# Kernel optimization log

Measured on AMD Instinct MI355X. Metric: run time of the kernel, lower is better.

The kernel has to match this reference:

```python
import jax, jax.numpy as jnp
import numpy as np

RARITY_ALPHA = 0.5


def _forward(obs_emb, observed_mask, lengths, avg_interval, var_prior_emb_tensor,
             rarity_W, adjI, p2s_W1, p2s_b1, p2s_W2, p2s_b2,
             Wu, bu, Wr, br, Wc, bc):
    B, T, N, D = obs_emb.shape
    I = jnp.eye(N, dtype=obs_emb.dtype)
    # hypernetwork conditioning vector per node (prior_to_state MLP); identical
    # across batch since var_prior_emb_tensor is repeated over the batch dim.
    vv = jax.nn.relu(var_prior_emb_tensor @ p2s_W1 + p2s_b1) @ p2s_W2 + p2s_b2  # [N,E]
    vv = jnp.broadcast_to(vv[None], (B, N, vv.shape[-1]))                        # [B,N,E]
    tot = observed_mask.sum(axis=1)  # var_total_obs [B,N]

    def gate(z, W, b):
        # MLP_Param: per-node weights W_n = sum_e vv[n,e]*W[e]; fused einsum avoids
        # materializing [B,N,2D+1,D].
        return jnp.einsum('bni,bne,eio->bno', z, vv, W) + jnp.einsum('bne,eo->bno', vv, b)

    def step_fn(carry, xs):
        h, out = carry
        cur_obs, m, cur_avg, step = xs  # [B,N,D], [B,N], [B,N], scalar
        rs = RARITY_ALPHA * jnp.tanh(cur_avg / (tot + 1.0))                  # [B,N]
        rmat = -rarity_W * jnp.abs(rs[:, :, None] - rs[:, None, :])          # [B,N,N]
        # adj_mask[b,i,j] = observed(b,i)*observed(b,j)  (column-set then row-zero)
        adj_mask = m[:, :, None] * m[:, None, :]
        cur_adj = adjI * (1.0 + rmat) * adj_mask * (1.0 - I) + I             # [B,N,N]
        x = jnp.concatenate([cur_obs, rs[..., None]], axis=-1)              # [B,N,D+1]
        comb = jnp.einsum('bij,bjf->bif', cur_adj,
                          jnp.concatenate([x, h], axis=-1))                  # [B,N,2D+1]
        r = jax.nn.sigmoid(gate(comb, Wr, br))
        u = jax.nn.sigmoid(gate(comb, Wu, bu))
        mm = m[..., None] > 0
        h1 = jnp.where(mm, r * h, h)                      # h[nodes_ind] = r*h[nodes_ind]
        cand = jnp.tanh(gate(jnp.concatenate([x, h1], axis=-1), Wc, bc))
        h2 = jnp.where(mm, (1.0 - u) * h1 + u * cand, h1)  # scatter back at observed nodes
        out = jnp.where((step == lengths - 1)[:, None, None], h2, out)
        return (h2, out), None

    h0 = jnp.zeros((B, N, D), obs_emb.dtype)
    xs = (obs_emb.transpose(1, 0, 2, 3), observed_mask.transpose(1, 0, 2),
          avg_interval.transpose(1, 0, 2), jnp.arange(T))
    (_, out), _ = jax.lax.scan(step_fn, (h0, jnp.zeros_like(h0)), xs)
    return out


def setup_inputs() -> dict:
    B, T, N, D, E = 32, 64, 128, 64, 5
    key = jax.random.key(0)
    ks = jax.random.split(key, 18)
    inp = {}
    inp['obs_emb'] = jax.random.normal(ks[0], (B, T, N, D), jnp.float32)
    inp['adj'] = jax.random.normal(ks[1], (N, N), jnp.float32)  # unused by forward
    inp['observed_mask'] = (jax.random.uniform(ks[2], (B, T, N)) < 0.5).astype(jnp.float32)
    inp['observed_tp'] = jax.random.uniform(ks[3], (B, T), jnp.float32)       # unused
    inp['tp_emb_tensor'] = jax.random.normal(ks[4], (B, T, 1), jnp.float32)   # unused
    inp['lengths'] = jax.random.randint(ks[5], (B,), T // 2, T + 1, jnp.int32)
    inp['avg_interval'] = jax.random.uniform(ks[6], (B, T, N), jnp.float32)
    inp['var_prior_emb_tensor'] = jax.random.normal(ks[7], (N, 768), jnp.float32)
    # learned parameters
    inp['rarity_W'] = jax.random.normal(ks[8], (N, N), jnp.float32)
    inp['adjI'] = jnp.eye(N, dtype=jnp.float32) + 0.01 * jax.random.normal(ks[9], (N, N), jnp.float32)
    inp['p2s_W1'] = 0.05 * jax.random.normal(ks[10], (768, 2 * D), jnp.float32)
    inp['p2s_b1'] = jnp.zeros((2 * D,), jnp.float32)
    inp['p2s_W2'] = 0.1 * jax.random.normal(ks[11], (2 * D, E), jnp.float32)
    inp['p2s_b2'] = jnp.zeros((E,), jnp.float32)
    inp['Wu'] = 0.1 * jax.random.normal(ks[12], (E, 2 * D + 1, D), jnp.float32)
    inp['bu'] = 0.1 * jax.random.normal(ks[13], (E, D), jnp.float32)
    inp['Wr'] = 0.1 * jax.random.normal(ks[14], (E, 2 * D + 1, D), jnp.float32)
    inp['br'] = 0.1 * jax.random.normal(ks[15], (E, D), jnp.float32)
    inp['Wc'] = 0.1 * jax.random.normal(ks[16], (E, 2 * D + 1, D), jnp.float32)
    inp['bc'] = 0.1 * jax.random.normal(ks[17], (E, D), jnp.float32)
    return inp


def reference(obs_emb, adj, observed_mask, observed_tp, tp_emb_tensor, lengths,
              avg_interval, var_prior_emb_tensor, rarity_W, adjI, p2s_W1, p2s_b1,
              p2s_W2, p2s_b2, Wu, bu, Wr, br, Wc, bc):
    # adj, observed_tp, tp_emb_tensor are accepted but never used, as in the torch code
    return _forward(obs_emb, observed_mask, lengths, avg_interval, var_prior_emb_tensor,
                    rarity_W, adjI, p2s_W1, p2s_b1, p2s_W2, p2s_b2,
                    Wu, bu, Wr, br, Wc, bc)
```

## Files before the change

kernel.cpp:

```cpp
#include <hip/hip_runtime.h>
#include <math.h>

constexpr size_t WS_VV  = 1024;
constexpr size_t WS_TOT = 2048;
constexpr size_t WS_RS  = 8192;
constexpr size_t WS_WH  = 270336;
constexpr size_t WS_WX  = 1843200;
constexpr size_t WS_BF  = 3440640;
constexpr size_t WS_H   = 3465216;
constexpr size_t CXSZ   = 2129920;
constexpr size_t GXSZ   = 2097152;
constexpr size_t WS_CX0 = 3727360;
constexpr size_t WS_GXR0= 7987200;
constexpr size_t WS_GXU0= 12181504;
constexpr size_t WS_CXC0= 16375808;

__device__ __forceinline__ float sigm(float x){ return 1.f/(1.f+expf(-x)); }

__device__ __forceinline__ float2 ld2_mall(const float* p){
  union { unsigned long long u; float2 f; } cv;
  cv.u = __hip_atomic_load((const unsigned long long*)p, __ATOMIC_RELAXED,
                           __HIP_MEMORY_SCOPE_AGENT);
  return cv.f;
}
__device__ __forceinline__ void st2_mall(float* p, float a, float b){
  union { unsigned long long u; float2 f; } cv;
  cv.f = make_float2(a, b);
  __hip_atomic_store((unsigned long long*)p, cv.u, __ATOMIC_RELAXED,
                     __HIP_MEMORY_SCOPE_AGENT);
}

__global__ void k_vv(const float* __restrict__ vpe, const float* __restrict__ W1,
                     const float* __restrict__ b1, const float* __restrict__ W2,
                     const float* __restrict__ b2, float* __restrict__ ws){
  int n = blockIdx.x, tid = threadIdx.x;
  __shared__ float hid[128];
  if (tid < 128){
    float acc = b1[tid];
    for (int k=0;k<768;k++) acc = fmaf(vpe[n*768+k], W1[k*128+tid], acc);
    hid[tid] = fmaxf(acc, 0.f);
  }
  __syncthreads();
  if (tid < 5){
    float acc = b2[tid];
    for (int h=0;h<128;h++) acc = fmaf(hid[h], W2[h*5+tid], acc);
    ws[WS_VV + n*5 + tid] = acc;
  }
}

__global__ void k_fold(const float* __restrict__ Wr, const float* __restrict__ Wu,
                       const float* __restrict__ Wc, const float* __restrict__ br,
                       const float* __restrict__ bu, const float* __restrict__ bc,
                       float* __restrict__ ws){
  int bid = blockIdx.x; int g = bid>>7; int n = bid&127;
  const float* W  = (g==0)?Wr:(g==1)?Wu:Wc;
  const float* bb = (g==0)?br:(g==1)?bu:bc;
  float v[5];
#pragma unroll
  for (int e=0;e<5;e++) v[e] = ws[WS_VV + n*5 + e];
  for (int idx=threadIdx.x; idx<129*64; idx+=256){
    int i = idx>>6, o = idx&63;
    float a = 0.f;
#pragma unroll
    for (int e=0;e<5;e++) a = fmaf(v[e], W[(e*129+i)*64+o], a);
    if (i < 65) ws[WS_WX + (size_t)(g*128+n)*4160 + i*64 + o] = a;
    else        ws[WS_WH + (size_t)(g*128+n)*4096 + (i-65)*64 + o] = a;
  }
  if (threadIdx.x < 64){
    int o = threadIdx.x; float a = 0.f;
#pragma unroll
    for (int e=0;e<5;e++) a = fmaf(v[e], bb[e*64+o], a);
    ws[WS_BF + (g*128+n)*64 + o] = a;
  }
}

__global__ void k_tot(const float* __restrict__ mask, float* __restrict__ ws){
  int id = blockIdx.x*256 + threadIdx.x;
  int b = id>>7, n = id&127;
  float s = 0.f;
  for (int t=0;t<64;t++) s += mask[(b*64+t)*128 + n];
  ws[WS_TOT + b*128 + n] = s;
}

__global__ void k_rs(const float* __restrict__ avg, float* __restrict__ ws){
  int id = blockIdx.x*256 + threadIdx.x;
  int b = id>>13, n = id&127;
  float tot = ws[WS_TOT + b*128 + n];
  ws[WS_RS + id] = 0.5f * tanhf(avg[id] / (tot + 1.f));
}

__device__ void p4a_body(float* smem, const float* __restrict__ obs,
      const float* __restrict__ mask, const float* __restrict__ adjI,
      const float* __restrict__ rW, const int* __restrict__ lengths,
      float* __restrict__ ws, int cc, int rc){
  int b = rc>>3, tl = rc&7, t = cc*8 + tl;
  if (t >= lengths[b]) return;
  int rt = b*64 + t;
  float* xt   = smem;
  float* adjh = smem + 4352;
  float* rs_l = smem + 13056;
  float* m_l  = smem + 13184;
  int tid = threadIdx.x;
  if (tid < 128){ rs_l[tid] = ws[WS_RS + rt*128 + tid]; m_l[tid] = mask[rt*128 + tid]; }
  __syncthreads();
  int it = tid>>3, ft = tid&7, i0 = it*4, f0 = ft*8;
  float4 aL[4], aH[4]; float a64[4];
#pragma unroll
  for (int ii=0;ii<4;ii++){ aL[ii]=make_float4(0,0,0,0); aH[ii]=make_float4(0,0,0,0); a64[ii]=0.f; }
  for (int half=0; half<2; half++){
    __syncthreads();
    int j0 = half*64;
    for (int idx=tid; idx<4096; idx+=256){
      int jl = idx>>6, f = idx&63;
      xt[jl*68+f] = obs[(size_t)rt*8192 + (j0+jl)*64 + f];
    }
    if (tid < 64) xt[tid*68+64] = rs_l[j0+tid];
    for (int idx=tid; idx<8192; idx+=256){
      int i = idx>>6, jl = idx&63, j = j0+jl;
      float a;
      if (i == j) a = 1.f;
      else {
        int gi = i*128 + j;
        float dd = fabsf(rs_l[i] - rs_l[j]);
        a = adjI[gi] * (1.f - rW[gi]*dd) * m_l[i] * m_l[j];
      }
      adjh[i*68+jl] = a;
    }
    __syncthreads();
    for (int jb=0; jb<16; jb++){
      float4 av[4];
#pragma unroll
      for (int ii=0;ii<4;ii++) av[ii] = *(const float4*)&adjh[(i0+ii)*68 + jb*4];
#pragma unroll
      for (int jj=0;jj<4;jj++){
        int jl = jb*4 + jj;
        float4 xlo = *(const float4*)&xt[jl*68 + f0];
        float4 xhi = *(const float4*)&xt[jl*68 + f0 + 4];
        float xr = xt[jl*68 + 64];
#pragma unroll
        for (int ii=0;ii<4;ii++){
          float a = (jj==0)?av[ii].x:(jj==1)?av[ii].y:(jj==2)?av[ii].z:av[ii].w;
          aL[ii].x = fmaf(a, xlo.x, aL[ii].x); aL[ii].y = fmaf(a, xlo.y, aL[ii].y);
          aL[ii].z = fmaf(a, xlo.z, aL[ii].z); aL[ii].w = fmaf(a, xlo.w, aL[ii].w);
          aH[ii].x = fmaf(a, xhi.x, aH[ii].x); aH[ii].y = fmaf(a, xhi.y, aH[ii].y);
          aH[ii].z = fmaf(a, xhi.z, aH[ii].z); aH[ii].w = fmaf(a, xhi.w, aH[ii].w);
          a64[ii] = fmaf(a, xr, a64[ii]);
        }
      }
    }
  }
  size_t cxb = WS_CX0 + (size_t)(cc&1)*CXSZ;
#pragma unroll
  for (int ii=0;ii<4;ii++){
    int i = i0 + ii;
    size_t base = cxb + (size_t)i*16640 + (size_t)rc*65 + f0;
    ws[base+0]=aL[ii].x; ws[base+1]=aL[ii].y; ws[base+2]=aL[ii].z; ws[base+3]=aL[ii].w;
    ws[base+4]=aH[ii].x; ws[base+5]=aH[ii].y; ws[base+6]=aH[ii].z; ws[base+7]=aH[ii].w;
    if (ft == 0) ws[cxb + (size_t)i*16640 + (size_t)rc*65 + 64] = a64[ii];
  }
}

__device__ void p4b_body(float* smem, const float* __restrict__ obs,
      const int* __restrict__ lengths, float* __restrict__ ws, int cc, int pbid){
  if (pbid >= 768) return;
  int g = pbid >> 8; int r2 = pbid & 255; int n = r2 >> 1; int tile = r2 & 1;
  float* A  = smem;
  float* Wl = smem + 8832;
  float* bl = smem + 12992;
  int* slen = (int*)(smem + 13056);
  int tid = threadIdx.x;
  if (tid < 32) slen[tid] = lengths[tid];
  for (int idx=tid; idx<4160; idx+=256) Wl[idx] = ws[WS_WX + (size_t)(g*128+n)*4160 + idx];
  if (tid < 64) bl[tid] = ws[WS_BF + (g*128+n)*64 + tid];
  size_t cxb = WS_CX0 + (size_t)(cc&1)*CXSZ;
  if (g < 2){
    const float* src = &ws[cxb + (size_t)n*16640 + (size_t)tile*8320];
    for (int idx=tid; idx<8320; idx+=256){
      int r = idx/65, f = idx - r*65;
      A[r*69+f] = src[idx];
    }
  } else {
    for (int idx=tid; idx<8320; idx+=256){
      int r = idx/65, f = idx - r*65;
      int grow = tile*128 + r;
      int gb = grow>>3, t = cc*8 + (grow&7);
      float v = (f < 64) ? obs[(size_t)(gb*64+t)*8192 + n*64 + f]
                         : ws[WS_RS + (gb*64+t)*128 + n];
      A[r*69+f] = v;
    }
  }
  __syncthreads();
  int rt8 = tid>>4, dq = tid&15;
  float4 acc[8];
#pragma unroll
  for (int rr=0;rr<8;rr++) acc[rr] = make_float4(0,0,0,0);
  for (int k=0;k<65;k++){
    float4 w = *(const float4*)&Wl[k*64 + dq*4];
#pragma unroll
    for (int rr=0;rr<8;rr++){
      float a = A[(rt8*8+rr)*69 + k];
      acc[rr].x = fmaf(a,w.x,acc[rr].x); acc[rr].y = fmaf(a,w.y,acc[rr].y);
      acc[rr].z = fmaf(a,w.z,acc[rr].z); acc[rr].w = fmaf(a,w.w,acc[rr].w);
    }
  }
  float4 b4 = *(const float4*)&bl[dq*4];
  size_t gxb = ((g==0)?WS_GXR0:(g==1)?WS_GXU0:WS_CXC0) + (size_t)(cc&1)*GXSZ;
#pragma unroll
  for (int rr=0;rr<8;rr++){
    int grow = tile*128 + rt8*8 + rr;
    int gb = grow>>3, gtl = grow&7;
    if (cc*8 + gtl < slen[gb]){
      float4 o; o.x=acc[rr].x+b4.x; o.y=acc[rr].y+b4.y; o.z=acc[rr].z+b4.z; o.w=acc[rr].w+b4.w;
      *(float4*)&ws[gxb + ((size_t)(n*8+gtl)*32 + gb)*64 + dq*4] = o;
    }
  }
}

__device__ void krec_body(float* smem, const float* __restrict__ mask,
      const int* __restrict__ lengths, const float* __restrict__ adjI,
      const float* __restrict__ rWm, float* __restrict__ out,
      float* __restrict__ ws, int c){
  __builtin_amdgcn_s_setprio(1);
  unsigned* hfl = (unsigned*)ws;
  const int bid = blockIdx.x, tid = threadIdx.x;
  const int bA = bid>>4, sl = bid&15, ns = sl*8;
  float* hs   = smem;
  float* adjT = smem + 8192;
  float* chT  = smem + 9216;
  float* hT   = smem + 9760;
  float* rs_l = smem + 10304;
  float* m_l  = smem + 10432;
  const int lenA = lengths[bA];
  const int ng = tid>>6, fA = tid&63;
  const int nl = (tid>>4)&7, fq = tid&15;
  const bool gthr = tid < 128;
  const int n  = ns + nl;
  float* hbuf = &ws[WS_H];
  const float* wrg = &ws[WS_WH + (size_t)(0*128+n)*4096];
  const float* wug = &ws[WS_WH + (size_t)(1*128+n)*4096];
  const float* wcg = &ws[WS_WH + (size_t)(2*128+n)*4096];
  const int c0 = c*8;
  const size_t gq = (size_t)(c&1)*GXSZ;

  for (int t=c0; t<c0+8; t++){
    if (t >= lenA){
      if (tid == 0)
        __hip_atomic_store(&hfl[bA*16+sl], (unsigned)(t+1), __ATOMIC_RELAXED,
                           __HIP_MEMORY_SCOPE_AGENT);
      __syncthreads();
      continue;
    }
    if (tid < 128) rs_l[tid] = ws[WS_RS + (size_t)(bA*64+t)*128 + tid];
    else           m_l[tid-128] = mask[(size_t)(bA*64+t)*128 + (tid-128)];
    __syncthreads();
    for (int idx=tid; idx<1024; idx+=256){
      int j = idx&127, il = idx>>7, I = ns+il;
      float a;
      if (I == j) a = 1.f;
      else {
        int gi = I*128 + j;
        float dd = fabsf(rs_l[I] - rs_l[j]);
        a = adjI[gi]*(1.f - rWm[gi]*dd)*m_l[I]*m_l[j];
      }
      adjT[j*8 + il] = a;
    }
    const int tl = t - c0;
    size_t gof = ((size_t)(n*8+tl)*32 + bA)*64 + fq*4;
    float4 arv = make_float4(0,0,0,0), auv = arv, acv = arv;
    if (gthr){
      arv = *(const float4*)&ws[WS_GXR0 + gq + gof];
      auv = *(const float4*)&ws[WS_GXU0 + gq + gof];
      acv = *(const float4*)&ws[WS_CXC0 + gq + gof];
    }
    const float msv = m_l[n];
    if (t > 0){
      if (tid < 16){
        unsigned tgt = (unsigned)t; int guard = 0;
        while (__hip_atomic_load(&hfl[bA*16 + tid], __ATOMIC_RELAXED,
                 __HIP_MEMORY_SCOPE_AGENT) < tgt && ++guard < (1<<20))
          __builtin_amdgcn_s_sleep(2);
      }
    }
    __syncthreads();
#pragma unroll
    for (int k=0;k<16;k++){
      int p = tid + 256*k;
      *(float2*)&hs[2*p] = ld2_mall(&hbuf[(size_t)bA*8192 + 2*p]);
    }
    __syncthreads();
    {
      float ac0 = 0.f, ac1 = 0.f;
#pragma unroll 4
      for (int j=0;j<128;j++){
        float hv = hs[j*64 + fA];
        float2 a2 = *(const float2*)&adjT[j*8 + ng*2];
        ac0 = fmaf(a2.x, hv, ac0);
        ac1 = fmaf(a2.y, hv, ac1);
      }
      chT[(ng*2+0)*68 + fA] = ac0;
      chT[(ng*2+1)*68 + fA] = ac1;
    }
    __syncthreads();
    float4 rr4, uu4, h1 = make_float4(0,0,0,0);
    if (gthr){
#pragma unroll 4
      for (int k=0;k<64;k++){
        float cv = chT[nl*68 + k];
        float4 wr4 = *(const float4*)&wrg[k*64 + fq*4];
        float4 wu4 = *(const float4*)&wug[k*64 + fq*4];
        arv.x = fmaf(cv,wr4.x,arv.x); arv.y = fmaf(cv,wr4.y,arv.y);
        arv.z = fmaf(cv,wr4.z,arv.z); arv.w = fmaf(cv,wr4.w,arv.w);
        auv.x = fmaf(cv,wu4.x,auv.x); auv.y = fmaf(cv,wu4.y,auv.y);
        auv.z = fmaf(cv,wu4.z,auv.z); auv.w = fmaf(cv,wu4.w,auv.w);
      }
      rr4.x = sigm(arv.x); rr4.y = sigm(arv.y); rr4.z = sigm(arv.z); rr4.w = sigm(arv.w);
      uu4.x = sigm(auv.x); uu4.y = sigm(auv.y); uu4.z = sigm(auv.z); uu4.w = sigm(auv.w);
      float4 hown = *(const float4*)&hs[n*64 + fq*4];
      bool ob = msv > 0.f;
      h1.x = ob ? rr4.x*hown.x : hown.x;
      h1.y = ob ? rr4.y*hown.y : hown.y;
      h1.z = ob ? rr4.z*hown.z : hown.z;
      h1.w = ob ? rr4.w*hown.w : hown.w;
      *(float4*)&hT[nl*68 + fq*4] = h1;
    }
    __syncthreads();
    if (gthr){
#pragma unroll 4
      for (int k=0;k<64;k++){
        float hv1 = hT[nl*68 + k];
        float4 wc4 = *(const float4*)&wcg[k*64 + fq*4];
        acv.x = fmaf(hv1,wc4.x,acv.x); acv.y = fmaf(hv1,wc4.y,acv.y);
        acv.z = fmaf(hv1,wc4.z,acv.z); acv.w = fmaf(hv1,wc4.w,acv.w);
      }
      float4 cd, h2;
      cd.x = tanhf(acv.x); cd.y = tanhf(acv.y); cd.z = tanhf(acv.z); cd.w = tanhf(acv.w);
      bool ob = msv > 0.f;
      h2.x = ob ? (1.f-uu4.x)*h1.x + uu4.x*cd.x : h1.x;
      h2.y = ob ? (1.f-uu4.y)*h1.y + uu4.y*cd.y : h1.y;
      h2.z = ob ? (1.f-uu4.z)*h1.z + uu4.z*cd.z : h1.z;
      h2.w = ob ? (1.f-uu4.w)*h1.w + uu4.w*cd.w : h1.w;
      float* hp = &hbuf[((size_t)bA*128 + n)*64 + fq*4];
      st2_mall(hp,   h2.x, h2.y);
      st2_mall(hp+2, h2.z, h2.w);
      if (t == lenA-1)
        *(float4*)&out[((size_t)bA*128 + n)*64 + fq*4] = h2;
    }
    __syncthreads();
    asm volatile("s_waitcnt vmcnt(0)" ::: "memory");
    if (tid == 0)
      __hip_atomic_store(&hfl[bA*16+sl], (unsigned)(t+1), __ATOMIC_RELAXED,
                         __HIP_MEMORY_SCOPE_AGENT);
  }
}

__global__ __launch_bounds__(256) void p4a_k(const float* __restrict__ obs,
      const float* __restrict__ mask, const float* __restrict__ adjI,
      const float* __restrict__ rW, const int* __restrict__ lengths,
      float* __restrict__ ws, int cc){
  __shared__ float smem[13312];
  p4a_body(smem, obs, mask, adjI, rW, lengths, ws, cc, blockIdx.x);
}
__global__ __launch_bounds__(256) void p4b_k(const float* __restrict__ obs,
      const int* __restrict__ lengths, float* __restrict__ ws, int cc){
  __shared__ float smem[13312];
  p4b_body(smem, obs, lengths, ws, cc, blockIdx.x);
}

__global__ __launch_bounds__(256) void kfused(const float* __restrict__ obs,
      const float* __restrict__ mask, const float* __restrict__ adjI,
      const float* __restrict__ rW, const int* __restrict__ lengths,
      float* __restrict__ out, float* __restrict__ ws, int c){
  __shared__ float smem[13312];
  int bid = blockIdx.x;
  if (bid < 512){
    krec_body(smem, mask, lengths, adjI, rW, out, ws, c);
    return;
  }
  bool has4a = (c < 6);
  if (has4a && bid < 768){
    p4a_body(smem, obs, mask, adjI, rW, lengths, ws, c+2, bid-512);
    return;
  }
  int pb = bid - (has4a ? 768 : 512);
  p4b_body(smem, obs, lengths, ws, c+1, pb);
}

extern "C" void kernel_launch(void* const* d_in, const int* in_sizes, int n_in,
                              void* d_out, int out_size, void* d_ws, size_t ws_size,
                              hipStream_t stream){
  const float* obs  = (const float*)d_in[0];
  const float* maskp= (const float*)d_in[2];
  const int*   lens = (const int*)d_in[5];
  const float* avg  = (const float*)d_in[6];
  const float* vpe  = (const float*)d_in[7];
  const float* rW   = (const float*)d_in[8];
  const float* adjI = (const float*)d_in[9];
  const float* W1   = (const float*)d_in[10];
  const float* b1   = (const float*)d_in[11];
  const float* W2   = (const float*)d_in[12];
  const float* b2   = (const float*)d_in[13];
  const float* Wu   = (const float*)d_in[14];
  const float* bu   = (const float*)d_in[15];
  const float* Wr   = (const float*)d_in[16];
  const float* br   = (const float*)d_in[17];
  const float* Wc   = (const float*)d_in[18];
  const float* bc   = (const float*)d_in[19];
  float* out = (float*)d_out;
  float* ws  = (float*)d_ws;
  hipMemsetAsync(d_ws, 0, 4096, stream);
  hipMemsetAsync((char*)d_ws + WS_H*sizeof(float), 0, 262144*sizeof(float), stream);
  k_vv  <<<128, 256, 0, stream>>>(vpe, W1, b1, W2, b2, ws);
  k_fold<<<384, 256, 0, stream>>>(Wr, Wu, Wc, br, bu, bc, ws);
  k_tot <<<16,  256, 0, stream>>>(maskp, ws);
  k_rs  <<<1024,256, 0, stream>>>(avg, ws);
  p4a_k<<<256, 256, 0, stream>>>(obs, maskp, adjI, rW, lens, ws, 0);
  p4a_k<<<256, 256, 0, stream>>>(obs, maskp, adjI, rW, lens, ws, 1);
  p4b_k<<<768, 256, 0, stream>>>(obs, lens, ws, 0);
  for (int c = 0; c < 8; c++){
    int grid = (c <= 5) ? 1536 : (c == 6) ? 1280 : 512;
    kfused<<<grid, 256, 0, stream>>>(obs, maskp, adjI, rW, lens, out, ws, c);
  }
}
```

Before: 1.462 ms.

## Split recurrent step into separate graph-combine and gate block roles with flag handoff

The recurrent block is split into two groups. 128 combine blocks compute adj·h per batch and quarter of the nodes and write it to a global buffer. 512 gate blocks each own one node for 8 batches, keep that node's three folded weight matrices resident in shared memory, and hold h in registers across steps. This removes the per-step re-reading of per-node gate weights from global memory. The cost is an extra global round-trip for the combined features and a two-way producer/consumer flag handshake between the block groups on every timestep, which adds latency and requires all of these blocks to be co-resident.

```diff
diff --git a/kernel.cpp b/kernel.cpp
--- a/kernel.cpp
+++ b/kernel.cpp
@@ -14,6 +14,7 @@
 constexpr size_t WS_GXR0= 7987200;
 constexpr size_t WS_GXU0= 12181504;
 constexpr size_t WS_CXC0= 16375808;
+constexpr size_t WS_CH  = 20570112;
 
 __device__ __forceinline__ float sigm(float x){ return 1.f/(1.f+expf(-x)); }
 
@@ -216,45 +217,125 @@
   }
 }
 
-__device__ void krec_body(float* smem, const float* __restrict__ mask,
-      const int* __restrict__ lengths, const float* __restrict__ adjI,
-      const float* __restrict__ rWm, float* __restrict__ out,
+__device__ void gate_body(float* smem, const float* __restrict__ mask,
+      const int* __restrict__ lengths, float* __restrict__ out,
       float* __restrict__ ws, int c){
   __builtin_amdgcn_s_setprio(1);
-  unsigned* hfl = (unsigned*)ws;
-  const int bid = blockIdx.x, tid = threadIdx.x;
-  const int bA = bid>>4, sl = bid&15, ns = sl*8;
+  unsigned* fH = (unsigned*)ws;
+  unsigned* fC = (unsigned*)ws + 512;
+  const int gid = blockIdx.x, tid = threadIdx.x;
+  const int n = gid >> 2, bq = gid & 3;
+  float* Wl  = smem;
+  float* chl = smem + 12288;
+  float* h1l = smem + 12816;
+  const int bl = tid >> 5, ln = tid & 31, f0 = ln*2;
+  const int b  = bq*8 + bl;
+  const int lenb = lengths[b];
+  float* hbuf = &ws[WS_H];
+  float* CH   = &ws[WS_CH];
+  const int c0 = c*8;
+  const size_t gq = (size_t)(c&1)*GXSZ;
+  for (int idx = tid; idx < 12288; idx += 256){
+    int g = idx >> 12, r = idx & 4095;
+    Wl[idx] = ws[WS_WH + ((size_t)(g*128+n))*4096 + r];
+  }
+  float2 hreg = ld2_mall(&hbuf[((size_t)b*128+n)*64 + f0]);
+  __syncthreads();
+  for (int t = c0; t < c0+8; t++){
+    const int tl = t - c0;
+    const bool alive = (t < lenb);
+    float msv = 0.f;
+    float2 arv = make_float2(0,0), auv = arv, acv = arv;
+    if (alive){
+      msv = mask[(size_t)(b*64+t)*128 + n];
+      size_t gof = ((size_t)(n*8+tl)*32 + b)*64 + f0;
+      arv = *(const float2*)&ws[WS_GXR0 + gq + gof];
+      auv = *(const float2*)&ws[WS_GXU0 + gq + gof];
+      acv = *(const float2*)&ws[WS_CXC0 + gq + gof];
+    }
+    if (tid < 32){
+      unsigned tgt = (unsigned)(t+1); int guard = 0;
+      while (__hip_atomic_load(&fC[(bq*8 + (tid>>2))*4 + (tid&3)], __ATOMIC_RELAXED,
+               __HIP_MEMORY_SCOPE_AGENT) < tgt && ++guard < (1<<20))
+        __builtin_amdgcn_s_sleep(2);
+    }
+    __syncthreads();
+    {
+      float2 v = ld2_mall(&CH[(size_t)n*2048 + b*64 + f0]);
+      chl[bl*66 + f0] = v.x; chl[bl*66 + f0 + 1] = v.y;
+    }
+    __syncthreads();
+#pragma unroll 4
+    for (int k=0;k<64;k++){
+      float cv = chl[bl*66 + k];
+      float2 wr = *(const float2*)&Wl[k*64 + f0];
+      float2 wu = *(const float2*)&Wl[4096 + k*64 + f0];
+      arv.x = fmaf(cv,wr.x,arv.x); arv.y = fmaf(cv,wr.y,arv.y);
+      auv.x = fmaf(cv,wu.x,auv.x); auv.y = fmaf(cv,wu.y,auv.y);
+    }
+    float2 r2, u2, h1;
+    r2.x = sigm(arv.x); r2.y = sigm(arv.y);
+    u2.x = sigm(auv.x); u2.y = sigm(auv.y);
+    bool ob = alive && (msv > 0.f);
+    h1.x = ob ? r2.x*hreg.x : hreg.x;
+    h1.y = ob ? r2.y*hreg.y : hreg.y;
+    h1l[bl*66 + f0] = h1.x; h1l[bl*66 + f0 + 1] = h1.y;
+    __syncthreads();
+#pragma unroll 4
+    for (int k=0;k<64;k++){
+      float hv = h1l[bl*66 + k];
+      float2 wc = *(const float2*)&Wl[8192 + k*64 + f0];
+      acv.x = fmaf(hv,wc.x,acv.x); acv.y = fmaf(hv,wc.y,acv.y);
+    }
+    float2 h2;
+    float cdx = tanhf(acv.x), cdy = tanhf(acv.y);
+    h2.x = ob ? (1.f-u2.x)*h1.x + u2.x*cdx : h1.x;
+    h2.y = ob ? (1.f-u2.y)*h1.y + u2.y*cdy : h1.y;
+    hreg = h2;
+    if (alive){
+      st2_mall(&hbuf[((size_t)b*128+n)*64 + f0], h2.x, h2.y);
+      if (t == lenb-1)
+        *(float2*)&out[((size_t)b*128+n)*64 + f0] = h2;
+    }
+    __syncthreads();
+    asm volatile("s_waitcnt vmcnt(0)" ::: "memory");
+    if (tid == 0)
+      __hip_atomic_store(&fH[bq*128 + n], (unsigned)(t+1), __ATOMIC_RELAXED,
+                         __HIP_MEMORY_SCOPE_AGENT);
+  }
+}
+
+__device__ void combh_body(float* smem, const float* __restrict__ mask,
+      const int* __restrict__ lengths, const float* __restrict__ adjI,
+      const float* __restrict__ rWm, float* __restrict__ ws, int c){
+  __builtin_amdgcn_s_setprio(1);
+  unsigned* fH = (unsigned*)ws;
+  unsigned* fC = (unsigned*)ws + 512;
+  const int cid = blockIdx.x - 512, tid = threadIdx.x;
+  const int b = cid >> 2, qt = cid & 3, I0 = qt*32;
+  const int bq = b >> 3;
   float* hs   = smem;
   float* adjT = smem + 8192;
-  float* chT  = smem + 9216;
-  float* hT   = smem + 9760;
-  float* rs_l = smem + 10304;
-  float* m_l  = smem + 10432;
-  const int lenA = lengths[bA];
-  const int ng = tid>>6, fA = tid&63;
-  const int nl = (tid>>4)&7, fq = tid&15;
-  const bool gthr = tid < 128;
-  const int n  = ns + nl;
+  float* rs_l = smem + 12800;
+  float* m_l  = smem + 12928;
+  const int lenb = lengths[b];
+  const int rg = tid >> 5, f2 = (tid & 31)*2;
   float* hbuf = &ws[WS_H];
-  const float* wrg = &ws[WS_WH + (size_t)(0*128+n)*4096];
-  const float* wug = &ws[WS_WH + (size_t)(1*128+n)*4096];
-  const float* wcg = &ws[WS_WH + (size_t)(2*128+n)*4096];
+  float* CH   = &ws[WS_CH];
   const int c0 = c*8;
-  const size_t gq = (size_t)(c&1)*GXSZ;
-
-  for (int t=c0; t<c0+8; t++){
-    if (t >= lenA){
+  for (int t = c0; t < c0+8; t++){
+    if (t >= lenb){
       if (tid == 0)
-        __hip_atomic_store(&hfl[bA*16+sl], (unsigned)(t+1), __ATOMIC_RELAXED,
+        __hip_atomic_store(&fC[b*4+qt], (unsigned)(t+1), __ATOMIC_RELAXED,
                            __HIP_MEMORY_SCOPE_AGENT);
       __syncthreads();
       continue;
     }
-    if (tid < 128) rs_l[tid] = ws[WS_RS + (size_t)(bA*64+t)*128 + tid];
-    else           m_l[tid-128] = mask[(size_t)(bA*64+t)*128 + (tid-128)];
-    __syncthreads();
-    for (int idx=tid; idx<1024; idx+=256){
-      int j = idx&127, il = idx>>7, I = ns+il;
+    if (tid < 128) rs_l[tid] = ws[WS_RS + (size_t)(b*64+t)*128 + tid];
+    else           m_l[tid-128] = mask[(size_t)(b*64+t)*128 + (tid-128)];
+    __syncthreads();
+    for (int idx = tid; idx < 4096; idx += 256){
+      int il = idx >> 7, j = idx & 127, I = I0 + il;
       float a;
       if (I == j) a = 1.f;
       else {
@@ -262,93 +343,40 @@
         float dd = fabsf(rs_l[I] - rs_l[j]);
         a = adjI[gi]*(1.f - rWm[gi]*dd)*m_l[I]*m_l[j];
       }
-      adjT[j*8 + il] = a;
-    }
-    const int tl = t - c0;
-    size_t gof = ((size_t)(n*8+tl)*32 + bA)*64 + fq*4;
-    float4 arv = make_float4(0,0,0,0), auv = arv, acv = arv;
-    if (gthr){
-      arv = *(const float4*)&ws[WS_GXR0 + gq + gof];
-      auv = *(const float4*)&ws[WS_GXU0 + gq + gof];
-      acv = *(const float4*)&ws[WS_CXC0 + gq + gof];
-    }
-    const float msv = m_l[n];
-    if (t > 0){
-      if (tid < 16){
-        unsigned tgt = (unsigned)t; int guard = 0;
-        while (__hip_atomic_load(&hfl[bA*16 + tid], __ATOMIC_RELAXED,
-                 __HIP_MEMORY_SCOPE_AGENT) < tgt && ++guard < (1<<20))
-          __builtin_amdgcn_s_sleep(2);
-      }
+      adjT[j*36 + il] = a;
+    }
+    if (t > 0 && tid < 128){
+      unsigned tgt = (unsigned)t; int guard = 0;
+      while (__hip_atomic_load(&fH[bq*128 + tid], __ATOMIC_RELAXED,
+               __HIP_MEMORY_SCOPE_AGENT) < tgt && ++guard < (1<<20))
+        __builtin_amdgcn_s_sleep(2);
     }
     __syncthreads();
 #pragma unroll
     for (int k=0;k<16;k++){
       int p = tid + 256*k;
-      *(float2*)&hs[2*p] = ld2_mall(&hbuf[(size_t)bA*8192 + 2*p]);
-    }
-    __syncthreads();
-    {
-      float ac0 = 0.f, ac1 = 0.f;
+      *(float2*)&hs[2*p] = ld2_mall(&hbuf[(size_t)b*8192 + 2*p]);
+    }
+    __syncthreads();
+    float2 acc[4] = {{0,0},{0,0},{0,0},{0,0}};
 #pragma unroll 4
-      for (int j=0;j<128;j++){
-        float hv = hs[j*64 + fA];
-        float2 a2 = *(const float2*)&adjT[j*8 + ng*2];
-        ac0 = fmaf(a2.x, hv, ac0);
-        ac1 = fmaf(a2.y, hv, ac1);
-      }
-      chT[(ng*2+0)*68 + fA] = ac0;
-      chT[(ng*2+1)*68 + fA] = ac1;
-    }
-    __syncthreads();
-    float4 rr4, uu4, h1 = make_float4(0,0,0,0);
-    if (gthr){
-#pragma unroll 4
-      for (int k=0;k<64;k++){
-        float cv = chT[nl*68 + k];
-        float4 wr4 = *(const float4*)&wrg[k*64 + fq*4];
-        float4 wu4 = *(const float4*)&wug[k*64 + fq*4];
-        arv.x = fmaf(cv,wr4.x,arv.x); arv.y = fmaf(cv,wr4.y,arv.y);
-        arv.z = fmaf(cv,wr4.z,arv.z); arv.w = fmaf(cv,wr4.w,arv.w);
-        auv.x = fmaf(cv,wu4.x,auv.x); auv.y = fmaf(cv,wu4.y,auv.y);
-        auv.z = fmaf(cv,wu4.z,auv.z); auv.w = fmaf(cv,wu4.w,auv.w);
-      }
-      rr4.x = sigm(arv.x); rr4.y = sigm(arv.y); rr4.z = sigm(arv.z); rr4.w = sigm(arv.w);
-      uu4.x = sigm(auv.x); uu4.y = sigm(auv.y); uu4.z = sigm(auv.z); uu4.w = sigm(auv.w);
-      float4 hown = *(const float4*)&hs[n*64 + fq*4];
-      bool ob = msv > 0.f;
-      h1.x = ob ? rr4.x*hown.x : hown.x;
-      h1.y = ob ? rr4.y*hown.y : hown.y;
-      h1.z = ob ? rr4.z*hown.z : hown.z;
-      h1.w = ob ? rr4.w*hown.w : hown.w;
-      *(float4*)&hT[nl*68 + fq*4] = h1;
-    }
-    __syncthreads();
-    if (gthr){
-#pragma unroll 4
-      for (int k=0;k<64;k++){
-        float hv1 = hT[nl*68 + k];
-        float4 wc4 = *(const float4*)&wcg[k*64 + fq*4];
-        acv.x = fmaf(hv1,wc4.x,acv.x); acv.y = fmaf(hv1,wc4.y,acv.y);
-        acv.z = fmaf(hv1,wc4.z,acv.z); acv.w = fmaf(hv1,wc4.w,acv.w);
-      }
-      float4 cd, h2;
-      cd.x = tanhf(acv.x); cd.y = tanhf(acv.y); cd.z = tanhf(acv.z); cd.w = tanhf(acv.w);
-      bool ob = msv > 0.f;
-      h2.x = ob ? (1.f-uu4.x)*h1.x + uu4.x*cd.x : h1.x;
-      h2.y = ob ? (1.f-uu4.y)*h1.y + uu4.y*cd.y : h1.y;
-      h2.z = ob ? (1.f-uu4.z)*h1.z + uu4.z*cd.z : h1.z;
-      h2.w = ob ? (1.f-uu4.w)*h1.w + uu4.w*cd.w : h1.w;
-      float* hp = &hbuf[((size_t)bA*128 + n)*64 + fq*4];
-      st2_mall(hp,   h2.x, h2.y);
-      st2_mall(hp+2, h2.z, h2.w);
-      if (t == lenA-1)
-        *(float4*)&out[((size_t)bA*128 + n)*64 + fq*4] = h2;
+    for (int j=0;j<128;j++){
+      float2 hv = *(const float2*)&hs[j*64 + f2];
+      float4 a4 = *(const float4*)&adjT[j*36 + rg*4];
+      acc[0].x = fmaf(a4.x,hv.x,acc[0].x); acc[0].y = fmaf(a4.x,hv.y,acc[0].y);
+      acc[1].x = fmaf(a4.y,hv.x,acc[1].x); acc[1].y = fmaf(a4.y,hv.y,acc[1].y);
+      acc[2].x = fmaf(a4.z,hv.x,acc[2].x); acc[2].y = fmaf(a4.z,hv.y,acc[2].y);
+      acc[3].x = fmaf(a4.w,hv.x,acc[3].x); acc[3].y = fmaf(a4.w,hv.y,acc[3].y);
+    }
+#pragma unroll
+    for (int rr=0;rr<4;rr++){
+      int n = I0 + rg*4 + rr;
+      st2_mall(&CH[(size_t)n*2048 + b*64 + f2], acc[rr].x, acc[rr].y);
     }
     __syncthreads();
     asm volatile("s_waitcnt vmcnt(0)" ::: "memory");
     if (tid == 0)
-      __hip_atomic_store(&hfl[bA*16+sl], (unsigned)(t+1), __ATOMIC_RELAXED,
+      __hip_atomic_store(&fC[b*4+qt], (unsigned)(t+1), __ATOMIC_RELAXED,
                          __HIP_MEMORY_SCOPE_AGENT);
   }
 }
@@ -357,12 +385,12 @@
       const float* __restrict__ mask, const float* __restrict__ adjI,
       const float* __restrict__ rW, const int* __restrict__ lengths,
       float* __restrict__ ws, int cc){
-  __shared__ float smem[13312];
+  __shared__ float smem[13344];
   p4a_body(smem, obs, mask, adjI, rW, lengths, ws, cc, blockIdx.x);
 }
 __global__ __launch_bounds__(256) void p4b_k(const float* __restrict__ obs,
       const int* __restrict__ lengths, float* __restrict__ ws, int cc){
-  __shared__ float smem[13312];
+  __shared__ float smem[13344];
   p4b_body(smem, obs, lengths, ws, cc, blockIdx.x);
 }
 
@@ -370,18 +398,22 @@
       const float* __restrict__ mask, const float* __restrict__ adjI,
       const float* __restrict__ rW, const int* __restrict__ lengths,
       float* __restrict__ out, float* __restrict__ ws, int c){
-  __shared__ float smem[13312];
+  __shared__ float smem[13344];
   int bid = blockIdx.x;
   if (bid < 512){
-    krec_body(smem, mask, lengths, adjI, rW, out, ws, c);
+    gate_body(smem, mask, lengths, out, ws, c);
     return;
   }
+  if (bid < 640){
+    combh_body(smem, mask, lengths, adjI, rW, ws, c);
+    return;
+  }
   bool has4a = (c < 6);
-  if (has4a && bid < 768){
-    p4a_body(smem, obs, mask, adjI, rW, lengths, ws, c+2, bid-512);
+  if (has4a && bid < 896){
+    p4a_body(smem, obs, mask, adjI, rW, lengths, ws, c+2, bid-640);
     return;
   }
-  int pb = bid - (has4a ? 768 : 512);
+  int pb = bid - (has4a ? 896 : 640);
   p4b_body(smem, obs, lengths, ws, c+1, pb);
 }
 
@@ -417,7 +449,7 @@
   p4a_k<<<256, 256, 0, stream>>>(obs, maskp, adjI, rW, lens, ws, 1);
   p4b_k<<<768, 256, 0, stream>>>(obs, lens, ws, 0);
   for (int c = 0; c < 8; c++){
-    int grid = (c <= 5) ? 1536 : (c == 6) ? 1280 : 512;
+    int grid = (c <= 5) ? 1664 : (c == 6) ? 1408 : 640;
     kfused<<<grid, 256, 0, stream>>>(obs, maskp, adjI, rW, lens, out, ws, c);
   }
 }
```

Result: no change. 1.482 ms (+1.4%).
